# Performance work log

Measured on AMD Instinct MI355X. Metric: run time of the kernel, lower is better.

## Reference

```python
import jax, jax.numpy as jnp
import numpy as np

N_NODES = 50000

def mpnn_layer(x, edge_index, edge_weight, Wm, Wu, bu):
    # x: [N, Din]; Wm, Wu: [Dout, Din]; bu: [Dout]
    src, dst = edge_index[0], edge_index[1]
    m = x @ Wm.T                                   # [N, Dout] linear message
    msg = edge_weight[:, None] * m[src]            # gather + weight  [E, Dout]
    agg = jax.ops.segment_sum(msg, dst, num_segments=N_NODES)  # scatter-add
    return jnp.tanh(x @ Wu.T + bu + agg)

def setup_inputs() -> dict:
    key = jax.random.key(0)
    ks = jax.random.split(key, 16)
    N, E, D_IN, H, OUT = N_NODES, 800000, 128, 128, 32
    inp = {
        'x': jax.random.normal(ks[0], (N, D_IN), dtype=jnp.float32),
        'edge_index': jax.random.randint(ks[1], (2, E), 0, N, dtype=jnp.int64),
        'edge_weight': jax.random.uniform(ks[2], (E,), dtype=jnp.float32),
    }
    scale = 0.05
    dims = [D_IN, H, H]  # per-layer input dims
    for l in range(3):
        inp[f'Wm{l}'] = jax.random.normal(ks[3 + 3 * l], (H, dims[l]), dtype=jnp.float32) * scale
        inp[f'Wu{l}'] = jax.random.normal(ks[4 + 3 * l], (H, dims[l]), dtype=jnp.float32) * scale
        inp[f'bu{l}'] = jnp.zeros((H,), dtype=jnp.float32)
    inp['Wout'] = jax.random.normal(ks[13], (OUT, H), dtype=jnp.float32) * scale
    inp['bout'] = jnp.zeros((OUT,), dtype=jnp.float32)
    return inp

def reference(x, edge_index, edge_weight, Wm0, Wu0, bu0, Wm1, Wu1, bu1, Wm2, Wu2, bu2, Wout, bout):
    h = x
    for Wm, Wu, bu in ((Wm0, Wu0, bu0), (Wm1, Wu1, bu1), (Wm2, Wu2, bu2)):
        h = mpnn_layer(h, edge_index, edge_weight, Wm, Wu, bu)
    return h @ Wout.T + bout
```

## Files before the change

kernel.cpp:

```cpp
#include <hip/hip_runtime.h>
#include <hip/hip_bf16.h>
#include <cstddef>


typedef __attribute__((ext_vector_type(8))) short short8;
typedef __attribute__((ext_vector_type(4))) float f32x4;
typedef unsigned short ushort_t;
typedef unsigned int uint_t;

#define BSH 8
#define BSZ 256
#define CAPB 6144
#define TSTRIDE 16
#define EPB 2048

__device__ inline ushort_t f2bf(float f) {
    uint_t u = __float_as_uint(f);
    uint_t r = u + 0x7FFFu + ((u >> 16) & 1u);
    return (ushort_t)(r >> 16);
}
__device__ inline float bf_lo(uint_t u) { return __uint_as_float(u << 16); }
__device__ inline float bf_hi(uint_t u) { return __uint_as_float(u & 0xFFFF0000u); }
__device__ inline uint_t packbf(float a, float b) {
    return (uint_t)f2bf(a) | ((uint_t)f2bf(b) << 16);
}

__device__ inline float fast_tanh(float x) {
    float e = __builtin_amdgcn_exp2f(x * 2.8853900817779268f);
    return 1.f - 2.f * __builtin_amdgcn_rcpf(e + 1.f);
}

__device__ inline int get_dst(const int* __restrict__ ei, int e, int E, int f) {
    if (f) return ei[E + e];
    return ((const int2*)ei)[(size_t)E + e].x;
}
__device__ inline int get_src(const int* __restrict__ ei, int e, int E, int f) {
    if (f) return ei[e];
    return ((const int2*)ei)[e].x;
}

struct SetupArgs {
    const float* Wm0; const float* Wu0;
    const float* Wm1; const float* Wu1;
    const float* Wm2; const float* Wu2;
    const float* Wout;
    const float* x; const int* ei;
    ushort_t* wswz;
    ushort_t* woswz;
    ushort_t* xb;
    int* tails;
    int* flag;
    int N, E, TI;
    int ZT, WB, XB;
};
__global__ __launch_bounds__(256) void setup_kernel(SetupArgs a) {
    int bx = blockIdx.x, t = threadIdx.x;
    if (bx < a.ZT) {
        int i = bx * 256 + t;
        if (i < a.TI) a.tails[i] = 0;
        return;
    }
    bx -= a.ZT;
    if (bx == 0) {
        __shared__ int any;
        if (t == 0) any = 0;
        __syncthreads();
        int n = a.E < 2048 ? a.E : 2048;
        for (int i = t; i < n; i += 256)
            if (a.ei[2 * i + 1] != 0) any = 1;
        __syncthreads();
        if (t == 0) a.flag[0] = any;
        return;
    }
    bx -= 1;
    if (bx < a.WB) {
        int i = bx * 256 + t;
        if (i < 3 * 32768) {
            int l = i >> 15, r2 = i & 32767;
            int ct = r2 >> 12, ks = (r2 >> 9) & 7, lane = (r2 >> 3) & 63, j = r2 & 7;
            int col = ct * 16 + (lane & 15);
            int k = ks * 32 + (lane >> 4) * 8 + j;
            const float* Wm = l == 0 ? a.Wm0 : (l == 1 ? a.Wm1 : a.Wm2);
            const float* Wu = l == 0 ? a.Wu0 : (l == 1 ? a.Wu1 : a.Wu2);
            float v = k < 128 ? Wm[col * 128 + k] : Wu[col * 128 + (k - 128)];
            a.wswz[(size_t)l * 32768 + r2] = f2bf(v);
        } else if (i < 3 * 32768 + 4096) {
            int r2 = i - 3 * 32768;
            int ct = r2 >> 11, ks = (r2 >> 9) & 3, lane = (r2 >> 3) & 63, j = r2 & 7;
            int col = ct * 16 + (lane & 15);
            int k = ks * 32 + (lane >> 4) * 8 + j;
            a.woswz[r2] = f2bf(a.Wout[col * 128 + k]);
        }
        return;
    }
    bx -= a.WB;
    {
        int j = bx * 256 + t;
        if (j < a.N * 32) {
            float4 v = *(const float4*)(a.x + (size_t)j * 4);
            uint2 o;
            o.x = packbf(v.x, v.y);
            o.y = packbf(v.z, v.w);
            *(uint2*)(a.xb + (size_t)j * 4) = o;
        }
    }
}

__global__ __launch_bounds__(256) void bin_kernel(
    const int* __restrict__ ei, const float* __restrict__ ew,
    const int* __restrict__ flag, int* __restrict__ tails,
    uint2* __restrict__ staged, int E, int NB) {
    __shared__ uint2 ent[EPB];
    __shared__ uint2 srt[EPB];
    __shared__ int cnt[256], cur[256], exc[256], runbase[256];
    const int tid = threadIdx.x;
    const int e0 = blockIdx.x * EPB;
    const int nE = (E - e0) < EPB ? (E - e0) : EPB;
    const int f = flag[0];
    cnt[tid] = 0;
    cur[tid] = 0;
    __syncthreads();
    for (int i = tid; i < nE; i += 256) {
        int e = e0 + i;
        int s = get_src(ei, e, E, f);
        int d = get_dst(ei, e, E, f);
        uint2 v;
        v.x = (uint_t)s | ((uint_t)f2bf(ew[e]) << 16);
        v.y = (uint_t)d;
        ent[i] = v;
        atomicAdd(&cnt[d >> BSH], 1);
    }
    __syncthreads();
    exc[tid] = cnt[tid];
    __syncthreads();
    for (int o = 1; o < 256; o <<= 1) {
        int v = tid >= o ? exc[tid - o] : 0;
        __syncthreads();
        exc[tid] += v;
        __syncthreads();
    }
    exc[tid] -= cnt[tid];
    if (tid < NB) {
        int c = cnt[tid];
        runbase[tid] = c ? atomicAdd(&tails[tid * TSTRIDE], c) : 0;
    }
    __syncthreads();
    for (int i = tid; i < nE; i += 256) {
        uint2 v = ent[i];
        int b = (int)(v.y >> BSH);
        int lp = atomicAdd(&cur[b], 1);
        srt[exc[b] + lp] = v;
    }
    __syncthreads();
    for (int i = tid; i < nE; i += 256) {
        uint2 v = srt[i];
        int b = (int)(v.y >> BSH);
        int gp = runbase[b] + (i - exc[b]);
        if (gp < CAPB) {
            uint2 o;
            o.x = v.x;
            o.y = (uint_t)(v.y & (BSZ - 1));
            staged[(size_t)b * CAPB + gp] = o;
        }
    }
}

__global__ __launch_bounds__(256) void place_kernel(
    const uint2* __restrict__ staged, const int* __restrict__ tails,
    int* __restrict__ cursor, uint_t* __restrict__ csr,
    int2* __restrict__ rowdeg, int N) {
    __shared__ int cnt[256], cur[256], excl[256], sm[256];
    __shared__ int baseSh;
    __shared__ uint_t outb[CAPB];
    const int b = blockIdx.x, tid = threadIdx.x;
    const int node0 = b << BSH;
    int tot = tails[b * TSTRIDE];
    tot = tot < CAPB ? tot : CAPB;
    cnt[tid] = 0;
    __syncthreads();
    const uint2* sp = staged + ((size_t)b * CAPB);
    for (int i = tid; i < tot; i += 256) atomicAdd(&cnt[sp[i].y], 1);
    __syncthreads();
    int c0 = cnt[tid];
    sm[tid] = c0;
    __syncthreads();
    for (int o = 1; o < 256; o <<= 1) {
        int v = tid >= o ? sm[tid - o] : 0;
        __syncthreads();
        sm[tid] += v;
        __syncthreads();
    }
    if (tid == 255) baseSh = atomicAdd(cursor, sm[255]);
    excl[tid] = sm[tid] - c0;
    cur[tid] = 0;
    __syncthreads();
    const int base = baseSh;
    for (int i = tid; i < tot; i += 256) {
        uint2 e = sp[i];
        int pos = excl[e.y] + atomicAdd(&cur[e.y], 1);
        outb[pos] = e.x;
    }
    __syncthreads();
    for (int i = tid; i < tot; i += 256) csr[base + i] = outb[i];
    if (node0 + tid < N) {
        int2 be;
        be.x = base + excl[tid];
        be.y = base + excl[tid] + c0;
        rowdeg[node0 + tid] = be;
    }
}

#define ACC16(W, V0, V1)                                         \
    do {                                                         \
        s[0] += (W) * bf_lo((V0).x);  s[1] += (W) * bf_hi((V0).x);  \
        s[2] += (W) * bf_lo((V0).y);  s[3] += (W) * bf_hi((V0).y);  \
        s[4] += (W) * bf_lo((V0).z);  s[5] += (W) * bf_hi((V0).z);  \
        s[6] += (W) * bf_lo((V0).w);  s[7] += (W) * bf_hi((V0).w);  \
        s[8] += (W) * bf_lo((V1).x);  s[9] += (W) * bf_hi((V1).x);  \
        s[10] += (W) * bf_lo((V1).y); s[11] += (W) * bf_hi((V1).y); \
        s[12] += (W) * bf_lo((V1).z); s[13] += (W) * bf_hi((V1).z); \
        s[14] += (W) * bf_lo((V1).w); s[15] += (W) * bf_hi((V1).w); \
    } while (0)

template <int WITH_OUT>
__global__ __launch_bounds__(256, 4) void fused_layer(
    const uint_t* __restrict__ csr, const int2* __restrict__ rowdeg,
    const ushort_t* __restrict__ h, const ushort_t* __restrict__ Wswz,
    const float* __restrict__ bias, ushort_t* __restrict__ Hout,
    const ushort_t* __restrict__ Woswz, const float* __restrict__ bout,
    float* __restrict__ Cout, int N) {
    __shared__ ushort_t Gt[16 * 128];
    __shared__ ushort_t Ht[16 * 128];
    const int tid = threadIdx.x;
    const int lane = tid & 63;
    const int wv = tid >> 6;
    const int R0 = blockIdx.x * 16;
    const int slot = lane >> 3, f8 = lane & 7;

    const int pp = tid * 16;
    const int srow = pp >> 8;
    const int sx = (pp & 255) ^ ((srow & 7) << 4);
    uint4 hst = *(const uint4*)(h + (size_t)(R0 + srow) * 128 + (sx >> 1));

#pragma unroll
    for (int i = 0; i < 4; ++i) {
        const int lr = wv * 4 + i;
        const int nd = R0 + lr;
        int beg = 0, end = 0;
        if (nd < N) { int2 be = rowdeg[nd]; beg = be.x; end = be.y; }
        float s[16];
#pragma unroll
        for (int k = 0; k < 16; ++k) s[k] = 0.f;
        for (int j = beg + slot; j < end; j += 32) {
            const int last = end - 1;
            const int j1 = (j + 8) < last ? (j + 8) : last;
            const int j2 = (j + 16) < last ? (j + 16) : last;
            const int j3 = (j + 24) < last ? (j + 24) : last;
            uint_t p0 = csr[j];
            uint_t p1 = csr[j1];
            uint_t p2 = csr[j2];
            uint_t p3 = csr[j3];
            const ushort_t* r0 = h + (size_t)(p0 & 0xFFFFu) * 128 + f8 * 16;
            const ushort_t* r1 = h + (size_t)(p1 & 0xFFFFu) * 128 + f8 * 16;
            const ushort_t* r2 = h + (size_t)(p2 & 0xFFFFu) * 128 + f8 * 16;
            const ushort_t* r3 = h + (size_t)(p3 & 0xFFFFu) * 128 + f8 * 16;
            uint4 a0 = *(const uint4*)(r0);
            uint4 a1 = *(const uint4*)(r0 + 8);
            uint4 b0 = *(const uint4*)(r1);
            uint4 b1 = *(const uint4*)(r1 + 8);
            uint4 c0 = *(const uint4*)(r2);
            uint4 c1 = *(const uint4*)(r2 + 8);
            uint4 d0 = *(const uint4*)(r3);
            uint4 d1 = *(const uint4*)(r3 + 8);
            float w0 = bf_hi(p0);
            float w1 = (j + 8) < end ? bf_hi(p1) : 0.f;
            float w2 = (j + 16) < end ? bf_hi(p2) : 0.f;
            float w3 = (j + 24) < end ? bf_hi(p3) : 0.f;
            ACC16(w0, a0, a1);
            ACC16(w1, b0, b1);
            ACC16(w2, c0, c1);
            ACC16(w3, d0, d1);
        }
#pragma unroll
        for (int k = 0; k < 16; ++k) s[k] += __shfl_xor(s[k], 8, 64);
#pragma unroll
        for (int k = 0; k < 16; ++k) s[k] += __shfl_xor(s[k], 16, 64);
#pragma unroll
        for (int k = 0; k < 16; ++k) s[k] += __shfl_xor(s[k], 32, 64);
        if (slot == 0) {
            uint4 o0, o1;
            o0.x = packbf(s[0], s[1]);   o0.y = packbf(s[2], s[3]);
            o0.z = packbf(s[4], s[5]);   o0.w = packbf(s[6], s[7]);
            o1.x = packbf(s[8], s[9]);   o1.y = packbf(s[10], s[11]);
            o1.z = packbf(s[12], s[13]); o1.w = packbf(s[14], s[15]);
            const int sw = (lr & 7) << 3;
            *(uint4*)(Gt + lr * 128 + ((f8 * 16) ^ sw)) = o0;
            *(uint4*)(Gt + lr * 128 + ((f8 * 16 + 8) ^ sw)) = o1;
        }
    }
    *(uint4*)((char*)Ht + pp) = hst;
    __syncthreads();

    const int m = lane & 15, kg = lane >> 4;
    const int lsw = (m & 7) << 3;
    const int colL = lane & 15, rq = lane >> 4;

    short8 b0f[8], b1f[8];
#pragma unroll
    for (int ksp = 0; ksp < 8; ++ksp) {
        b0f[ksp] = *(const short8*)(Wswz + (((2 * wv) * 8 + ksp) * 64 + lane) * 8);
        b1f[ksp] = *(const short8*)(Wswz + (((2 * wv + 1) * 8 + ksp) * 64 + lane) * 8);
    }
    const float bv0 = bias[(2 * wv) * 16 + colL];
    const float bv1 = bias[(2 * wv + 1) * 16 + colL];

    f32x4 acc0 = (f32x4){0.f, 0.f, 0.f, 0.f};
    f32x4 acc1 = (f32x4){0.f, 0.f, 0.f, 0.f};
#pragma unroll
    for (int ksp = 0; ksp < 8; ++ksp) {
        const ushort_t* tp = (ksp < 4) ? Gt : Ht;
        short8 av = *(const short8*)(tp + m * 128 + (((ksp & 3) * 32 + kg * 8) ^ lsw));
        acc0 = __builtin_amdgcn_mfma_f32_16x16x32_bf16(av, b0f[ksp], acc0, 0, 0, 0);
        acc1 = __builtin_amdgcn_mfma_f32_16x16x32_bf16(av, b1f[ksp], acc1, 0, 0, 0);
    }
    float v0[4], v1[4];
#pragma unroll
    for (int reg = 0; reg < 4; ++reg) {
        v0[reg] = fast_tanh(acc0[reg] + bv0);
        v1[reg] = fast_tanh(acc1[reg] + bv1);
    }

    if (WITH_OUT == 0) {
#pragma unroll
        for (int reg = 0; reg < 4; ++reg) {
            int gr = R0 + rq * 4 + reg;
            if (gr < N) {
                Hout[(size_t)gr * 128 + (2 * wv) * 16 + colL] = f2bf(v0[reg]);
                Hout[(size_t)gr * 128 + (2 * wv + 1) * 16 + colL] = f2bf(v1[reg]);
            }
        }
    } else {
        __syncthreads();
#pragma unroll
        for (int reg = 0; reg < 4; ++reg) {
            int lr3 = rq * 4 + reg;
            int sw3 = (lr3 & 7) << 3;
            Gt[lr3 * 128 + (((2 * wv) * 16 + colL) ^ sw3)] = f2bf(v0[reg]);
            Gt[lr3 * 128 + (((2 * wv + 1) * 16 + colL) ^ sw3)] = f2bf(v1[reg]);
        }
        __syncthreads();
        if (wv < 2) {
            const int oc = wv;
            const int osw = (m & 7) << 3;
            short8 ob[4];
#pragma unroll
            for (int ks = 0; ks < 4; ++ks)
                ob[ks] = *(const short8*)(Woswz + ((oc * 4 + ks) * 64 + lane) * 8);
            f32x4 oacc = (f32x4){0.f, 0.f, 0.f, 0.f};
#pragma unroll
            for (int ks = 0; ks < 4; ++ks) {
                short8 av = *(const short8*)(Gt + m * 128 + ((ks * 32 + kg * 8) ^ osw));
                oacc = __builtin_amdgcn_mfma_f32_16x16x32_bf16(av, ob[ks], oacc, 0, 0, 0);
            }
            const float obv = bout[oc * 16 + colL];
#pragma unroll
            for (int reg = 0; reg < 4; ++reg) {
                int gr = R0 + rq * 4 + reg;
                if (gr < N) Cout[(size_t)gr * 32 + oc * 16 + colL] = oacc[reg] + obv;
            }
        }
    }
}

extern "C" void kernel_launch(void* const* d_in, const int* in_sizes, int n_in,
                              void* d_out, int out_size, void* d_ws, size_t ws_size,
                              hipStream_t stream) {
    const float* x   = (const float*)d_in[0];
    const int* ei    = (const int*)d_in[1];
    const float* ew  = (const float*)d_in[2];
    const float* Wm[3] = {(const float*)d_in[3], (const float*)d_in[6], (const float*)d_in[9]};
    const float* Wu[3] = {(const float*)d_in[4], (const float*)d_in[7], (const float*)d_in[10]};
    const float* bu[3] = {(const float*)d_in[5], (const float*)d_in[8], (const float*)d_in[11]};
    const float* Wout = (const float*)d_in[12];
    const float* bout = (const float*)d_in[13];
    float* out = (float*)d_out;

    const int N = in_sizes[0] / 128;
    const int E = in_sizes[2];
    const size_t NPAD = 50048;
    const int NB = (N + BSZ - 1) / BSZ;
    const int TI = NB * TSTRIDE + 16;

    ushort_t* xb    = (ushort_t*)d_ws;
    ushort_t* hA    = xb + NPAD * 128;
    ushort_t* hB    = hA + NPAD * 128;
    ushort_t* gbuf  = hB + NPAD * 128;
    ushort_t* wswz  = gbuf + NPAD * 128;
    ushort_t* woswz = wswz + 3 * 32768;
    int* flag       = (int*)(woswz + 4096);
    int* tails      = flag + 1;
    int* cursor     = tails + NB * TSTRIDE;
    int* endp       = tails + TI;
    int2* rowdeg    = (int2*)(((uintptr_t)endp + 7) & ~(uintptr_t)7);
    uint2* staged   = (uint2*)(rowdeg + N + 8);
    uint_t* csr     = (uint_t*)(staged + (size_t)NB * CAPB);
    (void)ws_size;

    const int ZT = (TI + 255) / 256;
    const int WB = (3 * 32768 + 4096 + 255) / 256;
    const int XB = (N * 32 + 255) / 256;
    const int gB = (E + EPB - 1) / EPB;
    const int gF = (N + 15) / 16;

    SetupArgs sa;
    sa.Wm0 = Wm[0]; sa.Wu0 = Wu[0];
    sa.Wm1 = Wm[1]; sa.Wu1 = Wu[1];
    sa.Wm2 = Wm[2]; sa.Wu2 = Wu[2];
    sa.Wout = Wout; sa.x = x; sa.ei = ei;
    sa.wswz = wswz; sa.woswz = woswz; sa.xb = xb;
    sa.tails = tails; sa.flag = flag;
    sa.N = N; sa.E = E; sa.TI = TI;
    sa.ZT = ZT; sa.WB = WB; sa.XB = XB;
    setup_kernel<<<ZT + 1 + WB + XB, 256, 0, stream>>>(sa);

    bin_kernel<<<gB, 256, 0, stream>>>(ei, ew, flag, tails, staged, E, NB);
    place_kernel<<<NB, 256, 0, stream>>>(staged, tails, cursor, csr, rowdeg, N);

    fused_layer<0><<<gF, 256, 0, stream>>>(csr, rowdeg, xb, wswz, bu[0], hA,
                                           nullptr, nullptr, nullptr, N);
    fused_layer<0><<<gF, 256, 0, stream>>>(csr, rowdeg, hA, wswz + 32768, bu[1], hB,
                                           nullptr, nullptr, nullptr, N);
    fused_layer<1><<<gF, 256, 0, stream>>>(csr, rowdeg, hB, wswz + 2 * 32768, bu[2],
                                           nullptr, woswz, bout, out, N);
}
```

Before: 258.4 us.

## Restructure neighbor aggregation with shuffle-broadcast CSR entries and degree-specialized gathers

Each wave now preloads up to 32 CSR entries per row in one coalesced load, then broadcasts them with shuffles. It reorganizes lanes into 4 edge slots by 16 feature lanes, each handling 8 features instead of 16. Gathers are batched with a fast path for degree ≤16 (4 loads) and ≤32 (8 loads) and a tail loop for higher degrees. This cuts dependent CSR loads and raises memory-level parallelism for the average-degree-16 graph, at the cost of more shuffles and extra register arrays for the per-row accumulators.

```diff
diff --git a/kernel.cpp b/kernel.cpp
--- a/kernel.cpp
+++ b/kernel.cpp
@@ -7,6 +7,7 @@
 typedef __attribute__((ext_vector_type(4))) float f32x4;
 typedef unsigned short ushort_t;
 typedef unsigned int uint_t;
+typedef __attribute__((ext_vector_type(4))) uint_t u32x4;
 
 #define BSH 8
 #define BSZ 256
@@ -210,18 +211,6 @@
     }
 }
 
-#define ACC16(W, V0, V1)                                         \
-    do {                                                         \
-        s[0] += (W) * bf_lo((V0).x);  s[1] += (W) * bf_hi((V0).x);  \
-        s[2] += (W) * bf_lo((V0).y);  s[3] += (W) * bf_hi((V0).y);  \
-        s[4] += (W) * bf_lo((V0).z);  s[5] += (W) * bf_hi((V0).z);  \
-        s[6] += (W) * bf_lo((V0).w);  s[7] += (W) * bf_hi((V0).w);  \
-        s[8] += (W) * bf_lo((V1).x);  s[9] += (W) * bf_hi((V1).x);  \
-        s[10] += (W) * bf_lo((V1).y); s[11] += (W) * bf_hi((V1).y); \
-        s[12] += (W) * bf_lo((V1).z); s[13] += (W) * bf_hi((V1).z); \
-        s[14] += (W) * bf_lo((V1).w); s[15] += (W) * bf_hi((V1).w); \
-    } while (0)
-
 template <int WITH_OUT>
 __global__ __launch_bounds__(256, 4) void fused_layer(
     const uint_t* __restrict__ csr, const int2* __restrict__ rowdeg,
@@ -235,67 +224,99 @@
     const int lane = tid & 63;
     const int wv = tid >> 6;
     const int R0 = blockIdx.x * 16;
-    const int slot = lane >> 3, f8 = lane & 7;
+    const int sl = lane >> 4, fl = lane & 15;
 
     const int pp = tid * 16;
     const int srow = pp >> 8;
     const int sx = (pp & 255) ^ ((srow & 7) << 4);
     uint4 hst = *(const uint4*)(h + (size_t)(R0 + srow) * 128 + (sx >> 1));
 
+    int begs[4], degs[4];
+    uint_t cent[4];
 #pragma unroll
     for (int i = 0; i < 4; ++i) {
-        const int lr = wv * 4 + i;
-        const int nd = R0 + lr;
-        int beg = 0, end = 0;
-        if (nd < N) { int2 be = rowdeg[nd]; beg = be.x; end = be.y; }
-        float s[16];
-#pragma unroll
-        for (int k = 0; k < 16; ++k) s[k] = 0.f;
-        for (int j = beg + slot; j < end; j += 32) {
-            const int last = end - 1;
-            const int j1 = (j + 8) < last ? (j + 8) : last;
-            const int j2 = (j + 16) < last ? (j + 16) : last;
-            const int j3 = (j + 24) < last ? (j + 24) : last;
-            uint_t p0 = csr[j];
-            uint_t p1 = csr[j1];
-            uint_t p2 = csr[j2];
-            uint_t p3 = csr[j3];
-            const ushort_t* r0 = h + (size_t)(p0 & 0xFFFFu) * 128 + f8 * 16;
-            const ushort_t* r1 = h + (size_t)(p1 & 0xFFFFu) * 128 + f8 * 16;
-            const ushort_t* r2 = h + (size_t)(p2 & 0xFFFFu) * 128 + f8 * 16;
-            const ushort_t* r3 = h + (size_t)(p3 & 0xFFFFu) * 128 + f8 * 16;
-            uint4 a0 = *(const uint4*)(r0);
-            uint4 a1 = *(const uint4*)(r0 + 8);
-            uint4 b0 = *(const uint4*)(r1);
-            uint4 b1 = *(const uint4*)(r1 + 8);
-            uint4 c0 = *(const uint4*)(r2);
-            uint4 c1 = *(const uint4*)(r2 + 8);
-            uint4 d0 = *(const uint4*)(r3);
-            uint4 d1 = *(const uint4*)(r3 + 8);
-            float w0 = bf_hi(p0);
-            float w1 = (j + 8) < end ? bf_hi(p1) : 0.f;
-            float w2 = (j + 16) < end ? bf_hi(p2) : 0.f;
-            float w3 = (j + 24) < end ? bf_hi(p3) : 0.f;
-            ACC16(w0, a0, a1);
-            ACC16(w1, b0, b1);
-            ACC16(w2, c0, c1);
-            ACC16(w3, d0, d1);
-        }
-#pragma unroll
-        for (int k = 0; k < 16; ++k) s[k] += __shfl_xor(s[k], 8, 64);
-#pragma unroll
-        for (int k = 0; k < 16; ++k) s[k] += __shfl_xor(s[k], 16, 64);
-#pragma unroll
-        for (int k = 0; k < 16; ++k) s[k] += __shfl_xor(s[k], 32, 64);
-        if (slot == 0) {
-            uint4 o0, o1;
-            o0.x = packbf(s[0], s[1]);   o0.y = packbf(s[2], s[3]);
-            o0.z = packbf(s[4], s[5]);   o0.w = packbf(s[6], s[7]);
-            o1.x = packbf(s[8], s[9]);   o1.y = packbf(s[10], s[11]);
-            o1.z = packbf(s[12], s[13]); o1.w = packbf(s[14], s[15]);
-            const int sw = (lr & 7) << 3;
-            *(uint4*)(Gt + lr * 128 + ((f8 * 16) ^ sw)) = o0;
-            *(uint4*)(Gt + lr * 128 + ((f8 * 16 + 8) ^ sw)) = o1;
+        int nd = R0 + wv * 4 + i;
+        int bg = 0, dg = 0;
+        if (nd < N) { int2 be = rowdeg[nd]; bg = be.x; dg = be.y - be.x; }
+        begs[i] = bg; degs[i] = dg;
+        cent[i] = 0;
+        if (dg > 0) {
+            int idx = lane & 31;
+            idx = idx < dg ? idx : dg - 1;
+            cent[i] = csr[bg + idx];
+        }
+    }
+
+    float sacc[4][8];
+#pragma unroll
+    for (int i = 0; i < 4; ++i)
+#pragma unroll
+        for (int r = 0; r < 8; ++r) sacc[i][r] = 0.f;
+
+#pragma unroll
+    for (int i = 0; i < 4; ++i) {
+        uint_t pw[8];
+        const ushort_t* ra[8];
+#pragma unroll
+        for (int b = 0; b < 8; ++b) {
+            uint_t p = __shfl(cent[i], (b * 4 + sl) & 31, 64);
+            pw[b] = p;
+            ra[b] = h + (size_t)(p & 0xFFFFu) * 128 + fl * 8;
+        }
+        u32x4 v[8];
+        if (degs[i] > 16) {
+#pragma unroll
+            for (int b = 0; b < 8; ++b) v[b] = *(const u32x4*)ra[b];
+            __builtin_amdgcn_sched_group_barrier(0x020, 8, 0);
+#pragma unroll
+            for (int b = 0; b < 8; ++b) {
+                float w = ((b * 4 + sl) < degs[i]) ? bf_hi(pw[b]) : 0.f;
+                sacc[i][0] += w * bf_lo(v[b][0]); sacc[i][1] += w * bf_hi(v[b][0]);
+                sacc[i][2] += w * bf_lo(v[b][1]); sacc[i][3] += w * bf_hi(v[b][1]);
+                sacc[i][4] += w * bf_lo(v[b][2]); sacc[i][5] += w * bf_hi(v[b][2]);
+                sacc[i][6] += w * bf_lo(v[b][3]); sacc[i][7] += w * bf_hi(v[b][3]);
+            }
+        } else {
+#pragma unroll
+            for (int b = 0; b < 4; ++b) v[b] = *(const u32x4*)ra[b];
+            __builtin_amdgcn_sched_group_barrier(0x020, 4, 0);
+#pragma unroll
+            for (int b = 0; b < 4; ++b) {
+                float w = ((b * 4 + sl) < degs[i]) ? bf_hi(pw[b]) : 0.f;
+                sacc[i][0] += w * bf_lo(v[b][0]); sacc[i][1] += w * bf_hi(v[b][0]);
+                sacc[i][2] += w * bf_lo(v[b][1]); sacc[i][3] += w * bf_hi(v[b][1]);
+                sacc[i][4] += w * bf_lo(v[b][2]); sacc[i][5] += w * bf_hi(v[b][2]);
+                sacc[i][6] += w * bf_lo(v[b][3]); sacc[i][7] += w * bf_hi(v[b][3]);
+            }
+        }
+        if (degs[i] > 32) {
+            for (int j = begs[i] + 32 + sl; j < begs[i] + degs[i]; j += 4) {
+                uint_t p = csr[j];
+                float w = bf_hi(p);
+                u32x4 vv = *(const u32x4*)(h + (size_t)(p & 0xFFFFu) * 128 + fl * 8);
+                sacc[i][0] += w * bf_lo(vv[0]); sacc[i][1] += w * bf_hi(vv[0]);
+                sacc[i][2] += w * bf_lo(vv[1]); sacc[i][3] += w * bf_hi(vv[1]);
+                sacc[i][4] += w * bf_lo(vv[2]); sacc[i][5] += w * bf_hi(vv[2]);
+                sacc[i][6] += w * bf_lo(vv[3]); sacc[i][7] += w * bf_hi(vv[3]);
+            }
+        }
+    }
+
+#pragma unroll
+    for (int i = 0; i < 4; ++i) {
+#pragma unroll
+        for (int r = 0; r < 8; ++r) {
+            sacc[i][r] += __shfl_xor(sacc[i][r], 16, 64);
+            sacc[i][r] += __shfl_xor(sacc[i][r], 32, 64);
+        }
+        if (sl == 0) {
+            uint4 o;
+            o.x = packbf(sacc[i][0], sacc[i][1]);
+            o.y = packbf(sacc[i][2], sacc[i][3]);
+            o.z = packbf(sacc[i][4], sacc[i][5]);
+            o.w = packbf(sacc[i][6], sacc[i][7]);
+            const int lr = wv * 4 + i;
+            *(uint4*)(Gt + lr * 128 + ((fl * 8) ^ ((lr & 7) << 3))) = o;
         }
     }
     *(uint4*)((char*)Ht + pp) = hst;
```

Result: faster. 248.0 us (-4.1%).
